# Kernel tuning notes

Hardware: AMD Instinct MI355X
Metric: run time of the kernel (lower is better)

The kernel has to match this reference:

```python
import jax, jax.numpy as jnp
import numpy as np

NUM_SEGMENTS = 512
N = 200000
D = 256


def setup_inputs() -> dict:
    key = jax.random.key(0)
    k = jax.random.split(key, 6)
    x = jax.random.normal(k[0], (N, D), dtype=jnp.float32)
    batch = jnp.sort(jax.random.randint(k[1], (N,), 0, NUM_SEGMENTS))
    batch = batch.at[-1].set(NUM_SEGMENTS - 1)  # ensure batch.max()+1 == NUM_SEGMENTS
    W1 = jax.random.normal(k[2], (D, D // 2), dtype=jnp.float32) * (1.0 / np.sqrt(D))
    b1 = jax.random.normal(k[3], (D // 2,), dtype=jnp.float32) * 0.01
    W2 = jax.random.normal(k[4], (D // 2, 1), dtype=jnp.float32) * (1.0 / np.sqrt(D // 2))
    b2 = jax.random.normal(k[5], (1,), dtype=jnp.float32) * 0.01
    return {"x": x, "batch": batch, "W1": W1, "b1": b1, "W2": W2, "b2": b2}


def reference(x, batch, W1, b1, W2, b2):
    # attention MLP: Linear -> Tanh -> Linear -> [N, 1]
    scores = (jnp.tanh(x @ W1 + b1) @ W2 + b2)[:, 0]  # [N]
    # segment softmax (numerically stable): subtract per-segment max
    smax = jax.ops.segment_max(scores, batch, num_segments=NUM_SEGMENTS)  # [G]
    e = jnp.exp(scores - smax[batch])  # [N]
    denom = jax.ops.segment_sum(e, batch, num_segments=NUM_SEGMENTS)  # [G]
    denom = jnp.where(denom > 0, denom, 1.0)  # guard empty segments (original yields zeros)
    w = e / denom[batch]  # [N]
    # weighted sum pooling per segment -> [G, D]
    return jax.ops.segment_sum(x * w[:, None], batch, num_segments=NUM_SEGMENTS)
```

## Files before the change

kernel.cpp:

```cpp
#include <hip/hip_runtime.h>
#include <hip/hip_bf16.h>
#include <math.h>


typedef __attribute__((ext_vector_type(4))) float f32x4;
typedef __attribute__((ext_vector_type(8))) short s16x8;
typedef __attribute__((ext_vector_type(8))) unsigned short u16x8;

#define MFMA16(A, B, C) __builtin_amdgcn_mfma_f32_16x16x32_bf16((A), (B), (C), 0, 0, 0)

__device__ __forceinline__ unsigned short f2bf_rne(float f) {
    unsigned int u = __float_as_uint(f);
    unsigned int r = u + 0x7FFFu + ((u >> 16) & 1u);
    return (unsigned short)(r >> 16);
}
__device__ __forceinline__ float bf2f(unsigned short h) {
    return __uint_as_float(((unsigned int)h) << 16);
}

__global__ __launch_bounds__(256)
void prep_w1(const float* __restrict__ W1, unsigned short* __restrict__ bh,
             unsigned short* __restrict__ bl)
{
    for (int idx = blockIdx.x * 256 + threadIdx.x; idx < 128 * 256;
         idx += gridDim.x * 256) {
        int n = idx & 127, k = idx >> 7;
        float f = W1[(size_t)k * 128 + n];
        unsigned short h = f2bf_rne(f);
        bh[(size_t)n * 256 + k] = h;
        bl[(size_t)n * 256 + k] = f2bf_rne(f - bf2f(h));
    }
}

#define LPITCH 40

__global__ __launch_bounds__(256, 3)
void scores_mfma(const float* __restrict__ x,
                 const unsigned short* __restrict__ bh,
                 const unsigned short* __restrict__ bl,
                 const float* __restrict__ b1, const float* __restrict__ W2,
                 const float* __restrict__ b2, float* __restrict__ scores, int N)
{
    __shared__ __align__(16) unsigned short Ahi[128 * LPITCH];
    __shared__ __align__(16) unsigned short Alo[128 * LPITCH];
    __shared__ __align__(16) unsigned short Bhi[128 * LPITCH];
    __shared__ __align__(16) unsigned short Blo[128 * LPITCH];

    const int tid  = threadIdx.x;
    const int wave = tid >> 6;
    const int lane = tid & 63;
    const int c    = lane & 15;
    const int q    = lane >> 4;
    const int rowBase = blockIdx.x * 128;

    f32x4 acc[2][8];
#pragma unroll
    for (int mt = 0; mt < 2; ++mt)
#pragma unroll
        for (int nt = 0; nt < 8; ++nt)
            acc[mt][nt] = (f32x4){0.f, 0.f, 0.f, 0.f};

    const int arow  = rowBase + (tid >> 1);
    const int ak16  = (tid & 1) * 16;
    const int nB    = tid & 127;
    const int bk16  = (tid >> 7) * 16;

    f32x4 pa0, pa1, pa2, pa3;
    u16x8 pb0, pb1, pl0, pl1;

    auto loadA = [&](int k0) {
        if (arow < N) {
            const float* p = x + (size_t)arow * 256 + k0 + ak16;
            pa0 = *(const f32x4*)(p);
            pa1 = *(const f32x4*)(p + 4);
            pa2 = *(const f32x4*)(p + 8);
            pa3 = *(const f32x4*)(p + 12);
        } else {
            pa0 = pa1 = pa2 = pa3 = (f32x4){0.f, 0.f, 0.f, 0.f};
        }
    };
    auto loadB = [&](int k0) {
        const size_t base = (size_t)nB * 256 + k0 + bk16;
        pb0 = *(const u16x8*)(bh + base);
        pb1 = *(const u16x8*)(bh + base + 8);
        pl0 = *(const u16x8*)(bl + base);
        pl1 = *(const u16x8*)(bl + base + 8);
    };

    loadA(0);
    loadB(0);

    for (int it = 0; it < 8; ++it) {
        float af[16];
        *(f32x4*)&af[0]  = pa0; *(f32x4*)&af[4]  = pa1;
        *(f32x4*)&af[8]  = pa2; *(f32x4*)&af[12] = pa3;
        unsigned short ah[16], al[16];
#pragma unroll
        for (int j = 0; j < 8; ++j) {
            float a0 = af[2 * j], a1 = af[2 * j + 1];
            __hip_bfloat162 h2 = __float22bfloat162_rn(make_float2(a0, a1));
            ushort2 hu = *(ushort2*)&h2;
            float r0 = a0 - bf2f(hu.x), r1 = a1 - bf2f(hu.y);
            __hip_bfloat162 l2 = __float22bfloat162_rn(make_float2(r0, r1));
            ushort2 lu = *(ushort2*)&l2;
            ah[2 * j] = hu.x; ah[2 * j + 1] = hu.y;
            al[2 * j] = lu.x; al[2 * j + 1] = lu.y;
        }

        __syncthreads();
        {
            const int ar = tid >> 1;
            *(u16x8*)&Ahi[ar * LPITCH + ak16 + 0] = *(u16x8*)&ah[0];
            *(u16x8*)&Ahi[ar * LPITCH + ak16 + 8] = *(u16x8*)&ah[8];
            *(u16x8*)&Alo[ar * LPITCH + ak16 + 0] = *(u16x8*)&al[0];
            *(u16x8*)&Alo[ar * LPITCH + ak16 + 8] = *(u16x8*)&al[8];
            *(u16x8*)&Bhi[nB * LPITCH + bk16 + 0] = pb0;
            *(u16x8*)&Bhi[nB * LPITCH + bk16 + 8] = pb1;
            *(u16x8*)&Blo[nB * LPITCH + bk16 + 0] = pl0;
            *(u16x8*)&Blo[nB * LPITCH + bk16 + 8] = pl1;
        }
        __syncthreads();

        if (it < 7) {
            loadA((it + 1) * 32);
            loadB((it + 1) * 32);
        }

        s16x8 fah[2], fal[2];
#pragma unroll
        for (int mt = 0; mt < 2; ++mt) {
            int m = wave * 32 + mt * 16 + c;
            fah[mt] = *(const s16x8*)&Ahi[m * LPITCH + q * 8];
            fal[mt] = *(const s16x8*)&Alo[m * LPITCH + q * 8];
        }
#pragma unroll
        for (int nt = 0; nt < 8; ++nt) {
            int nr = nt * 16 + c;
            s16x8 fbh = *(const s16x8*)&Bhi[nr * LPITCH + q * 8];
            s16x8 fbl = *(const s16x8*)&Blo[nr * LPITCH + q * 8];
#pragma unroll
            for (int mt = 0; mt < 2; ++mt) {
                acc[mt][nt] = MFMA16(fah[mt], fbh, acc[mt][nt]);
                acc[mt][nt] = MFMA16(fah[mt], fbl, acc[mt][nt]);
                acc[mt][nt] = MFMA16(fal[mt], fbh, acc[mt][nt]);
            }
        }
    }

    float b1v[8], w2v[8];
#pragma unroll
    for (int nt = 0; nt < 8; ++nt) {
        b1v[nt] = b1[nt * 16 + c];
        w2v[nt] = W2[nt * 16 + c];
    }
    const float bias2 = b2[0];

#pragma unroll
    for (int mt = 0; mt < 2; ++mt) {
#pragma unroll
        for (int reg = 0; reg < 4; ++reg) {
            float p = 0.f;
#pragma unroll
            for (int nt = 0; nt < 8; ++nt) {
                float v = acc[mt][nt][reg] + b1v[nt];
                float e = __expf(2.f * v);
                p += (1.f - 2.f / (e + 1.f)) * w2v[nt];
            }
#pragma unroll
            for (int off = 8; off > 0; off >>= 1)
                p += __shfl_xor(p, off, 16);
            if (c == 0) {
                int row = rowBase + wave * 32 + mt * 16 + q * 4 + reg;
                if (row < N) scores[row] = p + bias2;
            }
        }
    }
}

__device__ __forceinline__ int lower_bound_dev(const int* __restrict__ b, int n, int v)
{
    int lo = 0, hi = n;
    while (lo < hi) {
        int mid = (lo + hi) >> 1;
        if (b[mid] < v) lo = mid + 1; else hi = mid;
    }
    return lo;
}

__global__ __launch_bounds__(1024)
void segpool_kernel(const float* __restrict__ x, const int* __restrict__ batch,
                    const float* __restrict__ scores, float* __restrict__ out, int N)
{
    const int g = blockIdx.x;
    const int tid = threadIdx.x;
    const int fidx  = tid & 63;
    const int rslot = tid >> 6;

    __shared__ int se[2];
    __shared__ float sred[1024];
    __shared__ float4 rbuf[16][64];

    if (tid < 2) se[tid] = lower_bound_dev(batch, N, g + tid);
    __syncthreads();
    const int start = se[0], end = se[1];

    float m = -INFINITY;
    for (int i = start + tid; i < end; i += 1024) m = fmaxf(m, scores[i]);
#pragma unroll
    for (int off = 32; off > 0; off >>= 1) m = fmaxf(m, __shfl_xor(m, off, 64));
    if ((tid & 63) == 0) sred[tid >> 6] = m;
    __syncthreads();
    if (tid < 16) {
        float v = sred[tid];
#pragma unroll
        for (int off = 8; off > 0; off >>= 1) v = fmaxf(v, __shfl_xor(v, off, 16));
        if (tid == 0) sred[0] = v;
    }
    __syncthreads();
    m = sred[0];
    __syncthreads();

    float ssum = 0.f;
    for (int i = start + tid; i < end; i += 1024) ssum += expf(scores[i] - m);
#pragma unroll
    for (int off = 32; off > 0; off >>= 1) ssum += __shfl_xor(ssum, off, 64);
    if ((tid & 63) == 0) sred[tid >> 6] = ssum;
    __syncthreads();
    if (tid < 16) {
        float v = sred[tid];
#pragma unroll
        for (int off = 8; off > 0; off >>= 1) v += __shfl_xor(v, off, 16);
        if (tid == 0) sred[0] = v;
    }
    __syncthreads();
    const float denom = sred[0];
    const float inv = (denom > 0.f) ? 1.f / denom : 0.f;

    float4 acc = make_float4(0.f, 0.f, 0.f, 0.f);
    for (int base = start; base < end; base += 1024) {
        int cnt = min(1024, end - base);
        __syncthreads();
        if (tid < cnt) sred[tid] = expf(scores[base + tid] - m) * inv;
        __syncthreads();
#pragma unroll 2
        for (int j = rslot; j < cnt; j += 16) {
            float w = sred[j];
            float4 v = *(const float4*)(x + (size_t)(base + j) * 256 + fidx * 4);
            acc.x = fmaf(w, v.x, acc.x);
            acc.y = fmaf(w, v.y, acc.y);
            acc.z = fmaf(w, v.z, acc.z);
            acc.w = fmaf(w, v.w, acc.w);
        }
    }

    rbuf[rslot][fidx] = acc;
    __syncthreads();
#pragma unroll
    for (int s = 8; s > 0; s >>= 1) {
        if (rslot < s) {
            float4 o = rbuf[rslot + s][fidx];
            acc.x += o.x; acc.y += o.y; acc.z += o.z; acc.w += o.w;
            rbuf[rslot][fidx] = acc;
        }
        __syncthreads();
    }
    if (rslot == 0)
        ((float4*)out)[(size_t)g * 64 + fidx] = acc;
}

extern "C" void kernel_launch(void* const* d_in, const int* in_sizes, int n_in,
                              void* d_out, int out_size, void* d_ws, size_t ws_size,
                              hipStream_t stream) {
    const float* x     = (const float*)d_in[0];
    const int*   batch = (const int*)  d_in[1];
    const float* W1    = (const float*)d_in[2];
    const float* b1    = (const float*)d_in[3];
    const float* W2    = (const float*)d_in[4];
    const float* b2    = (const float*)d_in[5];
    float* out = (float*)d_out;

    const int N = in_sizes[1];
    const int G = out_size / 256;

    float* scores = (float*)d_ws;

    unsigned short* bh = (unsigned short*)d_out;
    unsigned short* bl = bh + 128 * 256;

    prep_w1<<<64, 256, 0, stream>>>(W1, bh, bl);
    const int mblocks = (N + 127) / 128;
    scores_mfma<<<mblocks, 256, 0, stream>>>(x, bh, bl, b1, W2, b2, scores, N);
    segpool_kernel<<<G, 1024, 0, stream>>>(x, batch, scores, out, N);
}
```

Baseline: 363.5 us.

## Double-buffer GEMM A loads with priority scheduling and single-pass segment softmax pooling

The MLP GEMM kernel now keeps two register sets for x tiles, loading tiles up to three steps ahead. It uses explicit sched_barrier/s_barrier fences and raises wave priority around the MFMA block to overlap global loads and conversion with matrix math. The segment pooling kernel reads each segment's scores once into shared memory when the segment has at most 2048 rows, computes max and sum from registers, and defers the normalisation to one multiply at the end. Risks include higher register pressure from the extra buffers, and the manual waitcnt/barrier handling depending on correct ordering.

```diff
diff --git a/kernel.cpp b/kernel.cpp
--- a/kernel.cpp
+++ b/kernel.cpp
@@ -60,92 +60,114 @@
         for (int nt = 0; nt < 8; ++nt)
             acc[mt][nt] = (f32x4){0.f, 0.f, 0.f, 0.f};
 
-    const int arow  = rowBase + (tid >> 1);
-    const int ak16  = (tid & 1) * 16;
-    const int nB    = tid & 127;
-    const int bk16  = (tid >> 7) * 16;
-
-    f32x4 pa0, pa1, pa2, pa3;
+    const int arow = rowBase + (tid >> 1);
+    const int ak16 = (tid & 1) * 16;
+    const int nB   = tid & 127;
+    const int bk16 = (tid >> 7) * 16;
+    const int arsq = tid >> 1;
+    const bool aval = (arow < N);
+    const float* aptr = x + (size_t)arow * 256 + ak16;
+    const unsigned short* bhp = bh + (size_t)nB * 256 + bk16;
+    const unsigned short* blp = bl + (size_t)nB * 256 + bk16;
+
+    f32x4 Xa0, Xa1, Xa2, Xa3;
+    f32x4 Ya0, Ya1, Ya2, Ya3;
     u16x8 pb0, pb1, pl0, pl1;
 
-    auto loadA = [&](int k0) {
-        if (arow < N) {
-            const float* p = x + (size_t)arow * 256 + k0 + ak16;
-            pa0 = *(const f32x4*)(p);
-            pa1 = *(const f32x4*)(p + 4);
-            pa2 = *(const f32x4*)(p + 8);
-            pa3 = *(const f32x4*)(p + 12);
-        } else {
-            pa0 = pa1 = pa2 = pa3 = (f32x4){0.f, 0.f, 0.f, 0.f};
-        }
-    };
-    auto loadB = [&](int k0) {
-        const size_t base = (size_t)nB * 256 + k0 + bk16;
-        pb0 = *(const u16x8*)(bh + base);
-        pb1 = *(const u16x8*)(bh + base + 8);
-        pl0 = *(const u16x8*)(bl + base);
-        pl1 = *(const u16x8*)(bl + base + 8);
-    };
-
-    loadA(0);
-    loadB(0);
-
-    for (int it = 0; it < 8; ++it) {
-        float af[16];
-        *(f32x4*)&af[0]  = pa0; *(f32x4*)&af[4]  = pa1;
-        *(f32x4*)&af[8]  = pa2; *(f32x4*)&af[12] = pa3;
-        unsigned short ah[16], al[16];
-#pragma unroll
-        for (int j = 0; j < 8; ++j) {
-            float a0 = af[2 * j], a1 = af[2 * j + 1];
-            __hip_bfloat162 h2 = __float22bfloat162_rn(make_float2(a0, a1));
-            ushort2 hu = *(ushort2*)&h2;
-            float r0 = a0 - bf2f(hu.x), r1 = a1 - bf2f(hu.y);
-            __hip_bfloat162 l2 = __float22bfloat162_rn(make_float2(r0, r1));
-            ushort2 lu = *(ushort2*)&l2;
-            ah[2 * j] = hu.x; ah[2 * j + 1] = hu.y;
-            al[2 * j] = lu.x; al[2 * j + 1] = lu.y;
-        }
-
-        __syncthreads();
-        {
-            const int ar = tid >> 1;
-            *(u16x8*)&Ahi[ar * LPITCH + ak16 + 0] = *(u16x8*)&ah[0];
-            *(u16x8*)&Ahi[ar * LPITCH + ak16 + 8] = *(u16x8*)&ah[8];
-            *(u16x8*)&Alo[ar * LPITCH + ak16 + 0] = *(u16x8*)&al[0];
-            *(u16x8*)&Alo[ar * LPITCH + ak16 + 8] = *(u16x8*)&al[8];
-            *(u16x8*)&Bhi[nB * LPITCH + bk16 + 0] = pb0;
-            *(u16x8*)&Bhi[nB * LPITCH + bk16 + 8] = pb1;
-            *(u16x8*)&Blo[nB * LPITCH + bk16 + 0] = pl0;
-            *(u16x8*)&Blo[nB * LPITCH + bk16 + 8] = pl1;
-        }
-        __syncthreads();
-
-        if (it < 7) {
-            loadA((it + 1) * 32);
-            loadB((it + 1) * 32);
-        }
-
-        s16x8 fah[2], fal[2];
-#pragma unroll
-        for (int mt = 0; mt < 2; ++mt) {
-            int m = wave * 32 + mt * 16 + c;
-            fah[mt] = *(const s16x8*)&Ahi[m * LPITCH + q * 8];
-            fal[mt] = *(const s16x8*)&Alo[m * LPITCH + q * 8];
-        }
-#pragma unroll
-        for (int nt = 0; nt < 8; ++nt) {
-            int nr = nt * 16 + c;
-            s16x8 fbh = *(const s16x8*)&Bhi[nr * LPITCH + q * 8];
-            s16x8 fbl = *(const s16x8*)&Blo[nr * LPITCH + q * 8];
-#pragma unroll
-            for (int mt = 0; mt < 2; ++mt) {
-                acc[mt][nt] = MFMA16(fah[mt], fbh, acc[mt][nt]);
-                acc[mt][nt] = MFMA16(fah[mt], fbl, acc[mt][nt]);
-                acc[mt][nt] = MFMA16(fal[mt], fbh, acc[mt][nt]);
-            }
-        }
-    }
+#define LOADA(S, K0) do { \
+    if (aval) { const float* p_ = aptr + (K0); \
+        S##a0 = *(const f32x4*)(p_);     S##a1 = *(const f32x4*)(p_ + 4); \
+        S##a2 = *(const f32x4*)(p_ + 8); S##a3 = *(const f32x4*)(p_ + 12); } \
+    else { S##a0 = S##a1 = S##a2 = S##a3 = (f32x4){0.f, 0.f, 0.f, 0.f}; } } while (0)
+
+#define LOADB(K0) do { \
+    pb0 = *(const u16x8*)(bhp + (K0));     pb1 = *(const u16x8*)(bhp + (K0) + 8); \
+    pl0 = *(const u16x8*)(blp + (K0));     pl1 = *(const u16x8*)(blp + (K0) + 8); } while (0)
+
+#define CONVWRITE(S) do { \
+    float af_[16]; \
+    *(f32x4*)&af_[0]  = S##a0; *(f32x4*)&af_[4]  = S##a1; \
+    *(f32x4*)&af_[8]  = S##a2; *(f32x4*)&af_[12] = S##a3; \
+    unsigned short ah_[16], al_[16]; \
+    _Pragma("unroll") \
+    for (int j_ = 0; j_ < 8; ++j_) { \
+        float a0_ = af_[2*j_], a1_ = af_[2*j_+1]; \
+        __hip_bfloat162 h2_ = __float22bfloat162_rn(make_float2(a0_, a1_)); \
+        ushort2 hu_ = *(ushort2*)&h2_; \
+        float r0_ = a0_ - bf2f(hu_.x), r1_ = a1_ - bf2f(hu_.y); \
+        __hip_bfloat162 l2_ = __float22bfloat162_rn(make_float2(r0_, r1_)); \
+        ushort2 lu_ = *(ushort2*)&l2_; \
+        ah_[2*j_] = hu_.x; ah_[2*j_+1] = hu_.y; \
+        al_[2*j_] = lu_.x; al_[2*j_+1] = lu_.y; } \
+    *(u16x8*)&Ahi[arsq*LPITCH + ak16 + 0] = *(u16x8*)&ah_[0]; \
+    *(u16x8*)&Ahi[arsq*LPITCH + ak16 + 8] = *(u16x8*)&ah_[8]; \
+    *(u16x8*)&Alo[arsq*LPITCH + ak16 + 0] = *(u16x8*)&al_[0]; \
+    *(u16x8*)&Alo[arsq*LPITCH + ak16 + 8] = *(u16x8*)&al_[8]; \
+    *(u16x8*)&Bhi[nB*LPITCH + bk16 + 0] = pb0; \
+    *(u16x8*)&Bhi[nB*LPITCH + bk16 + 8] = pb1; \
+    *(u16x8*)&Blo[nB*LPITCH + bk16 + 0] = pl0; \
+    *(u16x8*)&Blo[nB*LPITCH + bk16 + 8] = pl1; } while (0)
+
+#define MFMA_ALL() do { \
+    s16x8 fah_[2], fal_[2]; \
+    _Pragma("unroll") \
+    for (int mt = 0; mt < 2; ++mt) { \
+        int m_ = wave * 32 + mt * 16 + c; \
+        fah_[mt] = *(const s16x8*)&Ahi[m_*LPITCH + q*8]; \
+        fal_[mt] = *(const s16x8*)&Alo[m_*LPITCH + q*8]; } \
+    _Pragma("unroll") \
+    for (int nt = 0; nt < 8; ++nt) { \
+        int nr_ = nt * 16 + c; \
+        s16x8 fbh_ = *(const s16x8*)&Bhi[nr_*LPITCH + q*8]; \
+        s16x8 fbl_ = *(const s16x8*)&Blo[nr_*LPITCH + q*8]; \
+        _Pragma("unroll") \
+        for (int mt = 0; mt < 2; ++mt) { \
+            acc[mt][nt] = MFMA16(fah_[mt], fbh_, acc[mt][nt]); \
+            acc[mt][nt] = MFMA16(fah_[mt], fbl_, acc[mt][nt]); \
+            acc[mt][nt] = MFMA16(fal_[mt], fbh_, acc[mt][nt]); } } } while (0)
+
+#define BARX() do { \
+    __builtin_amdgcn_sched_barrier(0); \
+    asm volatile("s_waitcnt lgkmcnt(0)" ::: "memory"); \
+    __builtin_amdgcn_s_barrier(); \
+    __builtin_amdgcn_sched_barrier(0); } while (0)
+
+#define PHASE(S, T) do { \
+    __builtin_amdgcn_s_setprio(1); \
+    MFMA_ALL(); \
+    __builtin_amdgcn_s_setprio(0); \
+    BARX(); \
+    CONVWRITE(S); \
+    if ((T) + 3 < 8) LOADA(S, 32 * ((T) + 3)); \
+    if ((T) + 2 < 8) LOADB(32 * ((T) + 2)); \
+    BARX(); } while (0)
+
+    LOADA(X, 0);
+    LOADB(0);
+    LOADA(Y, 32);
+    CONVWRITE(X);
+    LOADA(X, 64);
+    LOADB(32);
+    BARX();
+
+    PHASE(Y, 0);
+    PHASE(X, 1);
+    PHASE(Y, 2);
+    PHASE(X, 3);
+    PHASE(Y, 4);
+    PHASE(X, 5);
+    PHASE(Y, 6);
+
+    __builtin_amdgcn_s_setprio(1);
+    MFMA_ALL();
+    __builtin_amdgcn_s_setprio(0);
+
+#undef LOADA
+#undef LOADB
+#undef CONVWRITE
+#undef MFMA_ALL
+#undef BARX
+#undef PHASE
 
     float b1v[8], w2v[8];
 #pragma unroll
@@ -197,61 +219,119 @@
     const int rslot = tid >> 6;
 
     __shared__ int se[2];
-    __shared__ float sred[1024];
+    __shared__ float sred[16];
+    __shared__ float sw[2048];
     __shared__ float4 rbuf[16][64];
 
     if (tid < 2) se[tid] = lower_bound_dev(batch, N, g + tid);
     __syncthreads();
     const int start = se[0], end = se[1];
-
-    float m = -INFINITY;
-    for (int i = start + tid; i < end; i += 1024) m = fmaxf(m, scores[i]);
-#pragma unroll
-    for (int off = 32; off > 0; off >>= 1) m = fmaxf(m, __shfl_xor(m, off, 64));
-    if ((tid & 63) == 0) sred[tid >> 6] = m;
-    __syncthreads();
-    if (tid < 16) {
-        float v = sred[tid];
-#pragma unroll
-        for (int off = 8; off > 0; off >>= 1) v = fmaxf(v, __shfl_xor(v, off, 16));
-        if (tid == 0) sred[0] = v;
-    }
-    __syncthreads();
-    m = sred[0];
-    __syncthreads();
-
-    float ssum = 0.f;
-    for (int i = start + tid; i < end; i += 1024) ssum += expf(scores[i] - m);
-#pragma unroll
-    for (int off = 32; off > 0; off >>= 1) ssum += __shfl_xor(ssum, off, 64);
-    if ((tid & 63) == 0) sred[tid >> 6] = ssum;
-    __syncthreads();
-    if (tid < 16) {
-        float v = sred[tid];
-#pragma unroll
-        for (int off = 8; off > 0; off >>= 1) v += __shfl_xor(v, off, 16);
-        if (tid == 0) sred[0] = v;
-    }
-    __syncthreads();
-    const float denom = sred[0];
-    const float inv = (denom > 0.f) ? 1.f / denom : 0.f;
+    const int cnt = end - start;
 
     float4 acc = make_float4(0.f, 0.f, 0.f, 0.f);
-    for (int base = start; base < end; base += 1024) {
-        int cnt = min(1024, end - base);
-        __syncthreads();
-        if (tid < cnt) sred[tid] = expf(scores[base + tid] - m) * inv;
-        __syncthreads();
-#pragma unroll 2
+    float inv = 0.f;
+
+    if (cnt > 0 && cnt <= 2048) {
+        float s0 = (tid < cnt)        ? scores[start + tid]        : -INFINITY;
+        float s1 = (1024 + tid < cnt) ? scores[start + 1024 + tid] : -INFINITY;
+
+        float m = fmaxf(s0, s1);
+#pragma unroll
+        for (int off = 32; off > 0; off >>= 1) m = fmaxf(m, __shfl_xor(m, off, 64));
+        if ((tid & 63) == 0) sred[tid >> 6] = m;
+        __syncthreads();
+        if (tid < 16) {
+            float v = sred[tid];
+#pragma unroll
+            for (int off = 8; off > 0; off >>= 1) v = fmaxf(v, __shfl_xor(v, off, 16));
+            if (tid == 0) sred[0] = v;
+        }
+        __syncthreads();
+        m = sred[0];
+        __syncthreads();
+
+        float e0 = (tid < cnt)        ? __expf(s0 - m) : 0.f;
+        float e1 = (1024 + tid < cnt) ? __expf(s1 - m) : 0.f;
+        if (tid < cnt)        sw[tid] = e0;
+        if (1024 + tid < cnt) sw[1024 + tid] = e1;
+
+        float ss = e0 + e1;
+#pragma unroll
+        for (int off = 32; off > 0; off >>= 1) ss += __shfl_xor(ss, off, 64);
+        if ((tid & 63) == 0) sred[tid >> 6] = ss;
+        __syncthreads();
+        if (tid < 16) {
+            float v = sred[tid];
+#pragma unroll
+            for (int off = 8; off > 0; off >>= 1) v += __shfl_xor(v, off, 16);
+            if (tid == 0) sred[0] = v;
+        }
+        __syncthreads();
+        const float denom = sred[0];
+        inv = (denom > 0.f) ? 1.f / denom : 0.f;
+
+        const float* xg = x + (size_t)start * 256 + fidx * 4;
+#pragma unroll 4
         for (int j = rslot; j < cnt; j += 16) {
-            float w = sred[j];
-            float4 v = *(const float4*)(x + (size_t)(base + j) * 256 + fidx * 4);
+            float w = sw[j];
+            float4 v = *(const float4*)(xg + (size_t)j * 256);
             acc.x = fmaf(w, v.x, acc.x);
             acc.y = fmaf(w, v.y, acc.y);
             acc.z = fmaf(w, v.z, acc.z);
             acc.w = fmaf(w, v.w, acc.w);
         }
-    }
+    } else if (cnt > 2048) {
+        float m = -INFINITY;
+        for (int i = start + tid; i < end; i += 1024) m = fmaxf(m, scores[i]);
+#pragma unroll
+        for (int off = 32; off > 0; off >>= 1) m = fmaxf(m, __shfl_xor(m, off, 64));
+        if ((tid & 63) == 0) sred[tid >> 6] = m;
+        __syncthreads();
+        if (tid < 16) {
+            float v = sred[tid];
+#pragma unroll
+            for (int off = 8; off > 0; off >>= 1) v = fmaxf(v, __shfl_xor(v, off, 16));
+            if (tid == 0) sred[0] = v;
+        }
+        __syncthreads();
+        m = sred[0];
+        __syncthreads();
+
+        float ss = 0.f;
+        for (int i = start + tid; i < end; i += 1024) ss += __expf(scores[i] - m);
+#pragma unroll
+        for (int off = 32; off > 0; off >>= 1) ss += __shfl_xor(ss, off, 64);
+        if ((tid & 63) == 0) sred[tid >> 6] = ss;
+        __syncthreads();
+        if (tid < 16) {
+            float v = sred[tid];
+#pragma unroll
+            for (int off = 8; off > 0; off >>= 1) v += __shfl_xor(v, off, 16);
+            if (tid == 0) sred[0] = v;
+        }
+        __syncthreads();
+        const float denom = sred[0];
+        inv = (denom > 0.f) ? 1.f / denom : 0.f;
+
+        for (int base = start; base < end; base += 2048) {
+            int c2 = min(2048, end - base);
+            __syncthreads();
+            if (tid < c2)        sw[tid] = __expf(scores[base + tid] - m);
+            if (1024 + tid < c2) sw[1024 + tid] = __expf(scores[base + 1024 + tid] - m);
+            __syncthreads();
+            const float* xg = x + (size_t)base * 256 + fidx * 4;
+#pragma unroll 4
+            for (int j = rslot; j < c2; j += 16) {
+                float w = sw[j];
+                float4 v = *(const float4*)(xg + (size_t)j * 256);
+                acc.x = fmaf(w, v.x, acc.x);
+                acc.y = fmaf(w, v.y, acc.y);
+                acc.z = fmaf(w, v.z, acc.z);
+                acc.w = fmaf(w, v.w, acc.w);
+            }
+        }
+    }
+    acc.x *= inv; acc.y *= inv; acc.z *= inv; acc.w *= inv;
 
     rbuf[rslot][fidx] = acc;
     __syncthreads();
```

Measured after the change: 380.9 us. 4.8% more time.

## Fuse segment softmax pooling into score kernel with per-block partials and combine

Applied to the files above, without the earlier changes.

The scores kernel now keeps each tile's scores in shared memory and computes per-segment local max, exp-sum and weighted sums of x for the rows it just processed. It writes these partials to workspace. A light combine kernel merges them per segment with max-rescaling. This removes the second full pass over x (about 200 MB) and the scores round trip. The cost is extra shared memory, barriers and atomics in the GEMM kernel, and the assumption that a 128-row tile spans at most 4 segments.

```diff
diff --git a/kernel.cpp b/kernel.cpp
--- a/kernel.cpp
+++ b/kernel.cpp
@@ -8,6 +8,9 @@
 typedef __attribute__((ext_vector_type(8))) unsigned short u16x8;
 
 #define MFMA16(A, B, C) __builtin_amdgcn_mfma_f32_16x16x32_bf16((A), (B), (C), 0, 0, 0)
+
+#define MAXP 4
+#define PPITCH 260
 
 __device__ __forceinline__ unsigned short f2bf_rne(float f) {
     unsigned int u = __float_as_uint(f);
@@ -16,6 +19,13 @@
 }
 __device__ __forceinline__ float bf2f(unsigned short h) {
     return __uint_as_float(((unsigned int)h) << 16);
+}
+__device__ __forceinline__ unsigned fkey(float f) {
+    unsigned u = __float_as_uint(f);
+    return (u & 0x80000000u) ? ~u : (u | 0x80000000u);
+}
+__device__ __forceinline__ float funkey(unsigned k) {
+    return __uint_as_float((k & 0x80000000u) ? (k ^ 0x80000000u) : ~k);
 }
 
 __global__ __launch_bounds__(256)
@@ -35,16 +45,26 @@
 #define LPITCH 40
 
 __global__ __launch_bounds__(256, 3)
-void scores_mfma(const float* __restrict__ x,
+void scores_pool(const float* __restrict__ x,
                  const unsigned short* __restrict__ bh,
                  const unsigned short* __restrict__ bl,
                  const float* __restrict__ b1, const float* __restrict__ W2,
-                 const float* __restrict__ b2, float* __restrict__ scores, int N)
+                 const float* __restrict__ b2, const int* __restrict__ batch,
+                 float* __restrict__ partials, int N)
 {
     __shared__ __align__(16) unsigned short Ahi[128 * LPITCH];
     __shared__ __align__(16) unsigned short Alo[128 * LPITCH];
     __shared__ __align__(16) unsigned short Bhi[128 * LPITCH];
     __shared__ __align__(16) unsigned short Blo[128 * LPITCH];
+    __shared__ float sscore[128];
+    __shared__ int   sseg[128];
+    __shared__ float sew[128];
+    __shared__ int   pcnt[MAXP];
+    __shared__ int   pstart[MAXP + 1];
+    __shared__ unsigned pmaxu[MAXP];
+    __shared__ float pm[MAXP];
+    __shared__ float psum[MAXP];
+    __shared__ __align__(16) float4 redp[4][64];
 
     const int tid  = threadIdx.x;
     const int wave = tid >> 6;
@@ -169,11 +189,68 @@
 #pragma unroll
             for (int off = 8; off > 0; off >>= 1)
                 p += __shfl_xor(p, off, 16);
-            if (c == 0) {
-                int row = rowBase + wave * 32 + mt * 16 + q * 4 + reg;
-                if (row < N) scores[row] = p + bias2;
-            }
-        }
+            if (c == 0)
+                sscore[wave * 32 + mt * 16 + q * 4 + reg] = p + bias2;
+        }
+    }
+
+    const int nrows = min(128, N - rowBase);
+    if (tid < MAXP) { pcnt[tid] = 0; pmaxu[tid] = 0u; psum[tid] = 0.f; }
+    if (tid < nrows) sseg[tid] = batch[rowBase + tid];
+    __syncthreads();
+
+    const int seg0 = sseg[0];
+    const int npc  = min(sseg[nrows - 1] - seg0 + 1, MAXP);
+    int pp = 0;
+    if (tid < nrows) {
+        pp = min(sseg[tid] - seg0, MAXP - 1);
+        atomicAdd(&pcnt[pp], 1);
+        atomicMax(&pmaxu[pp], fkey(sscore[tid]));
+    }
+    __syncthreads();
+    if (tid == 0) {
+        int s = 0;
+#pragma unroll
+        for (int p2 = 0; p2 < MAXP; ++p2) { pstart[p2] = s; s += pcnt[p2]; }
+        pstart[MAXP] = s;
+    }
+    if (tid < MAXP) pm[tid] = funkey(pmaxu[tid]);
+    __syncthreads();
+    if (tid < nrows) {
+        float e = __expf(sscore[tid] - pm[pp]);
+        sew[tid] = e;
+        atomicAdd(&psum[pp], e);
+    }
+    __syncthreads();
+
+    const int fgrp  = tid & 63;
+    const int rslot = tid >> 6;
+    for (int p = 0; p < npc; ++p) {
+        const int r0 = pstart[p], r1 = pstart[p + 1];
+        if (r0 == r1) continue;
+        float4 pacc = make_float4(0.f, 0.f, 0.f, 0.f);
+        for (int r = r0 + rslot; r < r1; r += 4) {
+            float w = sew[r];
+            float4 v = *(const float4*)(x + (size_t)(rowBase + r) * 256 + fgrp * 4);
+            pacc.x = fmaf(w, v.x, pacc.x);
+            pacc.y = fmaf(w, v.y, pacc.y);
+            pacc.z = fmaf(w, v.z, pacc.z);
+            pacc.w = fmaf(w, v.w, pacc.w);
+        }
+        redp[rslot][fgrp] = pacc;
+        __syncthreads();
+        if (rslot == 0) {
+            float4 t0 = redp[0][fgrp], t1 = redp[1][fgrp];
+            float4 t2 = redp[2][fgrp], t3 = redp[3][fgrp];
+            t0.x += t1.x + t2.x + t3.x;
+            t0.y += t1.y + t2.y + t3.y;
+            t0.z += t1.z + t2.z + t3.z;
+            t0.w += t1.w + t2.w + t3.w;
+            float* P = partials + ((size_t)blockIdx.x * MAXP + p) * PPITCH;
+            ((float4*)P)[fgrp] = t0;
+            if (fgrp == 0) { P[256] = pm[p]; P[257] = psum[p]; }
+        }
+        __syncthreads();
     }
 }
 
@@ -187,85 +264,51 @@
     return lo;
 }
 
-__global__ __launch_bounds__(1024)
-void segpool_kernel(const float* __restrict__ x, const int* __restrict__ batch,
-                    const float* __restrict__ scores, float* __restrict__ out, int N)
+__global__ __launch_bounds__(256)
+void combine_kernel(const float* __restrict__ partials, const int* __restrict__ batch,
+                    float* __restrict__ out, int N)
 {
     const int g = blockIdx.x;
     const int tid = threadIdx.x;
-    const int fidx  = tid & 63;
-    const int rslot = tid >> 6;
-
-    __shared__ int se[2];
-    __shared__ float sred[1024];
-    __shared__ float4 rbuf[16][64];
-
-    if (tid < 2) se[tid] = lower_bound_dev(batch, N, g + tid);
-    __syncthreads();
-    const int start = se[0], end = se[1];
-
-    float m = -INFINITY;
-    for (int i = start + tid; i < end; i += 1024) m = fmaxf(m, scores[i]);
-#pragma unroll
-    for (int off = 32; off > 0; off >>= 1) m = fmaxf(m, __shfl_xor(m, off, 64));
-    if ((tid & 63) == 0) sred[tid >> 6] = m;
-    __syncthreads();
-    if (tid < 16) {
-        float v = sred[tid];
-#pragma unroll
-        for (int off = 8; off > 0; off >>= 1) v = fmaxf(v, __shfl_xor(v, off, 16));
-        if (tid == 0) sred[0] = v;
-    }
-    __syncthreads();
-    m = sred[0];
-    __syncthreads();
-
-    float ssum = 0.f;
-    for (int i = start + tid; i < end; i += 1024) ssum += expf(scores[i] - m);
-#pragma unroll
-    for (int off = 32; off > 0; off >>= 1) ssum += __shfl_xor(ssum, off, 64);
-    if ((tid & 63) == 0) sred[tid >> 6] = ssum;
-    __syncthreads();
-    if (tid < 16) {
-        float v = sred[tid];
-#pragma unroll
-        for (int off = 8; off > 0; off >>= 1) v += __shfl_xor(v, off, 16);
-        if (tid == 0) sred[0] = v;
-    }
-    __syncthreads();
-    const float denom = sred[0];
-    const float inv = (denom > 0.f) ? 1.f / denom : 0.f;
-
-    float4 acc = make_float4(0.f, 0.f, 0.f, 0.f);
-    for (int base = start; base < end; base += 1024) {
-        int cnt = min(1024, end - base);
-        __syncthreads();
-        if (tid < cnt) sred[tid] = expf(scores[base + tid] - m) * inv;
-        __syncthreads();
-#pragma unroll 2
-        for (int j = rslot; j < cnt; j += 16) {
-            float w = sred[j];
-            float4 v = *(const float4*)(x + (size_t)(base + j) * 256 + fidx * 4);
-            acc.x = fmaf(w, v.x, acc.x);
-            acc.y = fmaf(w, v.y, acc.y);
-            acc.z = fmaf(w, v.z, acc.z);
-            acc.w = fmaf(w, v.w, acc.w);
-        }
-    }
-
-    rbuf[rslot][fidx] = acc;
-    __syncthreads();
-#pragma unroll
-    for (int s = 8; s > 0; s >>= 1) {
-        if (rslot < s) {
-            float4 o = rbuf[rslot + s][fidx];
-            acc.x += o.x; acc.y += o.y; acc.z += o.z; acc.w += o.w;
-            rbuf[rslot][fidx] = acc;
-        }
-        __syncthreads();
-    }
-    if (rslot == 0)
-        ((float4*)out)[(size_t)g * 64 + fidx] = acc;
+    __shared__ int sse[2];
+    __shared__ int sslot[16];
+    __shared__ float sm[16], sscale[16];
+    __shared__ float sden;
+
+    if (tid < 2) sse[tid] = lower_bound_dev(batch, N, g + tid);
+    __syncthreads();
+    const int start = sse[0], end = sse[1];
+    if (start >= end) {
+        out[(size_t)g * 256 + tid] = 0.f;
+        return;
+    }
+    const int b0 = start >> 7, b1 = (end - 1) >> 7;
+    const int nb = min(b1 - b0 + 1, 16);
+
+    if (tid < nb) {
+        int b = b0 + tid;
+        int slot = min(g - batch[b << 7], MAXP - 1);
+        sslot[tid] = slot;
+        sm[tid] = partials[((size_t)b * MAXP + slot) * PPITCH + 256];
+    }
+    __syncthreads();
+    if (tid == 0) {
+        float M = -INFINITY;
+        for (int i = 0; i < nb; ++i) M = fmaxf(M, sm[i]);
+        float D = 0.f;
+        for (int i = 0; i < nb; ++i) {
+            float sc = __expf(sm[i] - M);
+            sscale[i] = sc;
+            D += sc * partials[((size_t)(b0 + i) * MAXP + sslot[i]) * PPITCH + 257];
+        }
+        sden = (D > 0.f) ? 1.f / D : 0.f;
+    }
+    __syncthreads();
+
+    float o = 0.f;
+    for (int i = 0; i < nb; ++i)
+        o += sscale[i] * partials[((size_t)(b0 + i) * MAXP + sslot[i]) * PPITCH + tid];
+    out[(size_t)g * 256 + tid] = o * sden;
 }
 
 extern "C" void kernel_launch(void* const* d_in, const int* in_sizes, int n_in,
@@ -282,13 +325,14 @@
     const int N = in_sizes[1];
     const int G = out_size / 256;
 
-    float* scores = (float*)d_ws;
+    float* partials = (float*)d_ws;
 
     unsigned short* bh = (unsigned short*)d_out;
     unsigned short* bl = bh + 128 * 256;
 
     prep_w1<<<64, 256, 0, stream>>>(W1, bh, bl);
     const int mblocks = (N + 127) / 128;
-    scores_mfma<<<mblocks, 256, 0, stream>>>(x, bh, bl, b1, W2, b2, scores, N);
-    segpool_kernel<<<G, 1024, 0, stream>>>(x, batch, scores, out, N);
-}
+    scores_pool<<<mblocks, 256, 0, stream>>>(x, bh, bl, b1, W2, b2, batch,
+                                             partials, N);
+    combine_kernel<<<G, 256, 0, stream>>>(partials, batch, out, N);
+}
```

Measured after the change: 364.4 us. No clear change (+0.2%).
